# Optimization experiments

Measured on AMD Instinct MI355X. Metric: run time of the kernel, lower is better.

The kernel has to match this reference:

```python
import jax, jax.numpy as jnp
import numpy as np

B, T, C, H, HS = 4, 2048, 1024, 16, 64
EPS = 1e-5


def setup_inputs() -> dict:
    key = jax.random.key(0)
    ks = jax.random.split(key, 16)
    s = lambda k, shp, fan: jax.random.normal(k, shp, jnp.float32) * (fan ** -0.5)
    return {
        "x": jax.random.normal(ks[0], (B, T, C), jnp.float32),
        "wq": s(ks[1], (H, C, HS), C), "bq": jnp.zeros((H, HS), jnp.float32),
        "wk": s(ks[2], (H, C, HS), C), "bk": jnp.zeros((H, HS), jnp.float32),
        "wv": s(ks[3], (H, C, HS), C), "bv": jnp.zeros((H, HS), jnp.float32),
        "wp": s(ks[4], (C, C), C), "bp": jnp.zeros((C,), jnp.float32),
        "w1": s(ks[5], (C, 4 * C), C), "b1": jnp.zeros((4 * C,), jnp.float32),
        "w2": s(ks[6], (4 * C, C), 4 * C), "b2": jnp.zeros((C,), jnp.float32),
        "g1": jnp.ones((C,), jnp.float32), "be1": jnp.zeros((C,), jnp.float32),
        "g2": jnp.ones((C,), jnp.float32), "be2": jnp.zeros((C,), jnp.float32),
    }


def _layernorm(x, g, b):
    mu = jnp.mean(x, axis=-1, keepdims=True)
    var = jnp.mean(jnp.square(x - mu), axis=-1, keepdims=True)
    return (x - mu) * jax.lax.rsqrt(var + EPS) * g + b


def reference(x, wq, bq, wk, bk, wv, bv, wp, bp, w1, b1, w2, b2, g1, be1, g2, be2):
    Bc, Tc, Cc = x.shape
    h = _layernorm(x, g1, be1)
    # per-head projections stacked: [B,H,T,HS]
    q = jnp.einsum('btc,hcd->bhtd', h, wq) + bq[None, :, None, :]
    k = jnp.einsum('btc,hcd->bhtd', h, wk) + bk[None, :, None, :]
    v = jnp.einsum('btc,hcd->bhtd', h, wv) + bv[None, :, None, :]
    # NOTE: source scales by 1/sqrt(n_embd), not 1/sqrt(head_size)
    scores = jnp.einsum('bhtd,bhsd->bhts', q, k) * (Cc ** -0.5)
    causal = jnp.tril(jnp.ones((Tc, Tc), bool))
    scores = jnp.where(causal, scores, -jnp.inf)
    attn = jax.nn.softmax(scores, axis=-1)
    out = jnp.einsum('bhts,bhsd->bhtd', attn, v)
    out = out.transpose(0, 2, 1, 3).reshape(Bc, Tc, Cc)  # concat heads
    x = x + out @ wp + bp
    h2 = _layernorm(x, g2, be2)
    ffn = jax.nn.relu(h2 @ w1 + b1) @ w2 + b2
    return x + ffn
```

## Files before the change

### kernel.cpp

```cpp
#include <hip/hip_runtime.h>


constexpr int Bb = 4, Tt = 2048, Cc = 1024, Hh = 16, HSz = 64, Ff = 4096;
constexpr int Mrows = Bb * Tt;

typedef __attribute__((ext_vector_type(8))) short bf16x8;
typedef __attribute__((ext_vector_type(4))) float f32x4;

__device__ __forceinline__ ushort f2bf(float f) {
  uint u = __builtin_bit_cast(uint, f);
  uint r = (u + 0x7fffu + ((u >> 16) & 1u)) >> 16;
  return (ushort)r;
}
__device__ __forceinline__ float bf2f(ushort s) {
  return __builtin_bit_cast(float, ((uint)s) << 16);
}
__device__ __forceinline__ uint cvtpk_bf16(float lo, float hi) {
  uint r;
  asm("v_cvt_pk_bf16_f32 %0, %1, %2" : "=v"(r) : "v"(lo), "v"(hi));
  return r;
}
__device__ __forceinline__ void gload16(const void* g, void* l) {
  __builtin_amdgcn_global_load_lds(
      (const __attribute__((address_space(1))) void*)g,
      (__attribute__((address_space(3))) void*)l, 16, 0, 0);
}

__global__ __launch_bounds__(256) void ln_kernel(const float* __restrict__ x,
                                                 const float* __restrict__ g,
                                                 const float* __restrict__ b,
                                                 ushort* __restrict__ out) {
  int row = blockIdx.x;
  const float* xr = x + (size_t)row * Cc;
  int c4 = threadIdx.x * 4;
  float4 v = *(const float4*)(xr + c4);
  float s1 = v.x + v.y + v.z + v.w;
  float s2 = v.x * v.x + v.y * v.y + v.z * v.z + v.w * v.w;
#pragma unroll
  for (int off = 32; off >= 1; off >>= 1) {
    s1 += __shfl_xor(s1, off);
    s2 += __shfl_xor(s2, off);
  }
  __shared__ float red[8];
  int wid = threadIdx.x >> 6, lane = threadIdx.x & 63;
  if (lane == 0) { red[wid] = s1; red[4 + wid] = s2; }
  __syncthreads();
  float t1 = red[0] + red[1] + red[2] + red[3];
  float t2 = red[4] + red[5] + red[6] + red[7];
  float mu = t1 * (1.0f / Cc);
  float var = t2 * (1.0f / Cc) - mu * mu;
  float rs = rsqrtf(var + 1e-5f);
  float4 gv = *(const float4*)(g + c4);
  float4 bv = *(const float4*)(b + c4);
  ushort4 o;
  o.x = f2bf((v.x - mu) * rs * gv.x + bv.x);
  o.y = f2bf((v.y - mu) * rs * gv.y + bv.y);
  o.z = f2bf((v.z - mu) * rs * gv.z + bv.z);
  o.w = f2bf((v.w - mu) * rs * gv.w + bv.w);
  *(ushort4*)(out + (size_t)row * Cc + c4) = o;
}

__device__ __forceinline__ void tcast_body(const float* __restrict__ src,
                                           ushort* __restrict__ dst, int ldS,
                                           int ldD, int r0, int c0) {
  __shared__ float t[32][33];
  int c = threadIdx.x & 31, r8 = threadIdx.x >> 5;
#pragma unroll
  for (int i = 0; i < 4; ++i) {
    int r = r8 + i * 8;
    t[r][c] = src[(size_t)(r0 + r) * ldS + c0 + c];
  }
  __syncthreads();
#pragma unroll
  for (int i = 0; i < 4; ++i) {
    int rr = r8 + i * 8;
    dst[(size_t)(c0 + rr) * ldD + r0 + c] = f2bf(t[c][rr]);
  }
}

__global__ __launch_bounds__(256) void tcast_kernel(const float* __restrict__ src,
                                                    ushort* __restrict__ dst,
                                                    int ldS, int ldD) {
  tcast_body(src, dst, ldS, ldD, blockIdx.x * 32, blockIdx.y * 32);
}

__global__ __launch_bounds__(256) void tcast_qkv(const float* __restrict__ wq,
                                                 const float* __restrict__ wk,
                                                 const float* __restrict__ wv,
                                                 ushort* __restrict__ dst) {
  int z = blockIdx.z, zz = z >> 4, h = z & 15;
  const float* src = (zz == 0 ? wq : (zz == 1 ? wk : wv)) + (size_t)h * Cc * HSz;
  ushort* d = dst + (size_t)(zz * 1024 + h * 64) * 1024;
  tcast_body(src, d, HSz, Cc, blockIdx.x * 32, blockIdx.y * 32);
}

__global__ __launch_bounds__(256) void bias_concat(const float* __restrict__ bq,
                                                   const float* __restrict__ bk,
                                                   const float* __restrict__ bv,
                                                   float* __restrict__ dst) {
  int i = blockIdx.x * 256 + threadIdx.x;
  dst[i] = i < 1024 ? bq[i] : (i < 2048 ? bk[i - 1024] : bv[i - 2048]);
}

__device__ __forceinline__ void gemm_main(const ushort* __restrict__ A, int lda,
                                          const ushort* __restrict__ Bt, int ldb,
                                          int K, int m0, int n0,
                                          ushort* __restrict__ As,
                                          ushort* __restrict__ Bs,
                                          f32x4 (&acc)[4][2]) {
  int tid = threadIdx.x, wid = tid >> 6, lane = tid & 63;
  int wr = wid >> 2, wc = wid & 3, fr = lane & 15, fq = lane >> 4;
  const ushort* Ag = A + (size_t)m0 * lda;
  const ushort* Bg = Bt + (size_t)n0 * ldb;
  for (int k0 = 0; k0 < K; k0 += 64) {
#pragma unroll
    for (int c = 0; c < 2; ++c) {
      int slot = c * 512 + tid;
      int row = slot >> 3, s = slot & 7;
      int sw = (s << 3) ^ ((row & 7) << 3);
      gload16(Ag + (size_t)row * lda + k0 + sw, As + (size_t)(c * 512 + wid * 64) * 8);
      gload16(Bg + (size_t)row * ldb + k0 + sw, Bs + (size_t)(c * 512 + wid * 64) * 8);
    }
    __syncthreads();
    bf16x8 av[4][2], bv[2][2];
#pragma unroll
    for (int m = 0; m < 4; ++m) {
      int row = wr * 64 + m * 16 + fr;
#pragma unroll
      for (int ks = 0; ks < 2; ++ks)
        av[m][ks] = *(const bf16x8*)&As[row * 64 + (((ks * 4 + fq) ^ (row & 7)) << 3)];
    }
#pragma unroll
    for (int n = 0; n < 2; ++n) {
      int row = wc * 32 + n * 16 + fr;
#pragma unroll
      for (int ks = 0; ks < 2; ++ks)
        bv[n][ks] = *(const bf16x8*)&Bs[row * 64 + (((ks * 4 + fq) ^ (row & 7)) << 3)];
    }
#pragma unroll
    for (int m = 0; m < 4; ++m)
#pragma unroll
      for (int n = 0; n < 2; ++n)
#pragma unroll
        for (int ks = 0; ks < 2; ++ks)
          acc[m][n] = __builtin_amdgcn_mfma_f32_16x16x32_bf16(
              av[m][ks], bv[n][ks], acc[m][n], 0, 0, 0);
    __syncthreads();
  }
}

__device__ __forceinline__ void xcd_swz(int& bx, int& by) {
  int bid = blockIdx.x + blockIdx.y * gridDim.x;
  int cpx = (gridDim.x * gridDim.y) >> 3;
  int id = (bid & 7) * cpx + (bid >> 3);
  bx = id % gridDim.x;
  by = id / gridDim.x;
}

template <bool RELU, bool HASRES, bool OUTBF16>
__global__ __launch_bounds__(512) void gemm_bf16(
    const ushort* __restrict__ A, int lda, const ushort* __restrict__ Bt,
    int ldb, const float* __restrict__ bias, const float* __restrict__ res,
    void* __restrict__ Cout, int ldc, int K) {
  __shared__ __align__(16) ushort As[128 * 64];
  __shared__ __align__(16) ushort Bs[128 * 64];
  f32x4 acc[4][2] = {};
  int bx, by;
  xcd_swz(bx, by);
  int m0 = by * 128, n0 = bx * 128;
  gemm_main(A, lda, Bt, ldb, K, m0, n0, As, Bs, acc);
  int lane = threadIdx.x & 63, wid = threadIdx.x >> 6;
  int wr = wid >> 2, wc = wid & 3, fr = lane & 15, fq = lane >> 4;
#pragma unroll
  for (int m = 0; m < 4; ++m) {
    int gm = m0 + wr * 64 + m * 16 + fq * 4;
#pragma unroll
    for (int n = 0; n < 2; ++n) {
      int gn = n0 + wc * 32 + n * 16 + fr;
      float bsv = bias[gn];
#pragma unroll
      for (int j = 0; j < 4; ++j) {
        int row = gm + j;
        float v = acc[m][n][j] + bsv;
        if constexpr (HASRES) v += res[(size_t)row * ldc + gn];
        if constexpr (RELU) v = fmaxf(v, 0.f);
        if constexpr (OUTBF16)
          ((ushort*)Cout)[(size_t)row * ldc + gn] = f2bf(v);
        else
          ((float*)Cout)[(size_t)row * ldc + gn] = v;
      }
    }
  }
}

__global__ __launch_bounds__(512) void gemm_qkv(const ushort* __restrict__ A,
                                                const ushort* __restrict__ Bt,
                                                const float* __restrict__ bias,
                                                ushort* __restrict__ q,
                                                ushort* __restrict__ k,
                                                ushort* __restrict__ vt) {
  __shared__ __align__(16) ushort As[128 * 64];
  __shared__ __align__(16) ushort Bs[128 * 64];
  f32x4 acc[4][2] = {};
  int bx, by;
  xcd_swz(bx, by);
  int m0 = by * 128, n0 = bx * 128;
  gemm_main(A, 1024, Bt, 1024, 1024, m0, n0, As, Bs, acc);
  int lane = threadIdx.x & 63, wid = threadIdx.x >> 6;
  int wr = wid >> 2, wc = wid & 3, fr = lane & 15, fq = lane >> 4;
  const float qscale = 1.4426950408889634f / 32.0f;
#pragma unroll
  for (int m = 0; m < 4; ++m) {
    int gm = m0 + wr * 64 + m * 16 + fq * 4;
#pragma unroll
    for (int n = 0; n < 2; ++n) {
      int gn = n0 + wc * 32 + n * 16 + fr;
      float bsv = bias[gn];
      if (gn < 1024) {
#pragma unroll
        for (int j = 0; j < 4; ++j)
          q[(size_t)(gm + j) * 1024 + gn] = f2bf((acc[m][n][j] + bsv) * qscale);
      } else if (gn < 2048) {
        int col = gn - 1024;
#pragma unroll
        for (int j = 0; j < 4; ++j)
          k[(size_t)(gm + j) * 1024 + col] = f2bf(acc[m][n][j] + bsv);
      } else {
        int dd = gn - 2048, h = dd >> 6, d = dd & 63;
        int bbr = gm >> 11, t = gm & 2047;
        ushort4 pw = {f2bf(acc[m][n][0] + bsv), f2bf(acc[m][n][1] + bsv),
                      f2bf(acc[m][n][2] + bsv), f2bf(acc[m][n][3] + bsv)};
        *(ushort4*)&vt[(((size_t)(bbr * 16 + h)) * 64 + d) * 2048 + t] = pw;
      }
    }
  }
}

constexpr int QB = 128, KVB = 64;
__global__ __launch_bounds__(512) void attn_kernel(const ushort* __restrict__ Qb,
                                                   const ushort* __restrict__ Kb,
                                                   const ushort* __restrict__ Vt,
                                                   ushort* __restrict__ att) {
  __shared__ __align__(16) ushort Klds[2][64 * 64];
  __shared__ __align__(16) ushort Vlds[2][64 * 64];
  __shared__ __align__(16) ushort Plds[8][16 * 64];
  int tid = threadIdx.x, wid = tid >> 6, lane = tid & 63;
  int fr = lane & 15, fq = lane >> 4;
  int bh = blockIdx.y, bb = bh >> 4, hh = bh & 15;
  const ushort* qkbase = Qb + ((size_t)bb * Tt) * Cc + hh * HSz;
  const ushort* Kbase = Kb + ((size_t)bb * Tt) * Cc + hh * HSz;
  const ushort* Vbase = Vt + ((size_t)(bb * Hh + hh)) * HSz * Tt;
  int srow = tid >> 3;
  int ssw = ((tid & 7) << 3) ^ ((srow & 7) << 3);

#pragma unroll 1
  for (int pass = 0; pass < 2; ++pass) {
    int qt = pass ? (Tt / QB - 1 - (int)blockIdx.x) : (int)blockIdx.x;
    int q0 = qt * QB;
    int q0w = q0 + wid * 16;

    bf16x8 Qreg[2];
#pragma unroll
    for (int d2 = 0; d2 < 2; ++d2)
      Qreg[d2] = *(const bf16x8*)(qkbase + (size_t)(q0w + fr) * Cc + d2 * 32 + fq * 8);
    f32x4 Oa[4] = {};
    float mrow = -1e30f, lrow = 0.f;
    int nt = q0 / KVB + 2;

    __syncthreads();
    gload16(Kbase + (size_t)srow * Cc + ssw, (char*)Klds[0] + wid * 1024);
    gload16(Vbase + (size_t)srow * Tt + ssw, (char*)Vlds[0] + wid * 1024);

#pragma unroll 1
    for (int kt = 0; kt < nt; ++kt) {
      int t0 = kt * KVB;
      int c = kt & 1;
      __syncthreads();
      if (kt + 1 < nt) {
        int t0n = t0 + KVB;
        gload16(Kbase + (size_t)(t0n + srow) * Cc + ssw,
                (char*)Klds[c ^ 1] + wid * 1024);
        gload16(Vbase + (size_t)srow * Tt + t0n + ssw,
                (char*)Vlds[c ^ 1] + wid * 1024);
      }
      if (q0w + 15 < t0) continue;

      const char* Kc = (const char*)Klds[c];
      const char* Vc = (const char*)Vlds[c];
      bf16x8 kf[4][2];
#pragma unroll
      for (int ks = 0; ks < 4; ++ks)
#pragma unroll
        for (int d2 = 0; d2 < 2; ++d2) {
          int row = ks * 16 + fr;
          int off = (d2 * 64 + fq * 16) ^ ((row & 7) << 4);
          kf[ks][d2] = *(const bf16x8*)(Kc + row * 128 + off);
        }
      f32x4 accs[4] = {};
      __builtin_amdgcn_s_setprio(1);
#pragma unroll
      for (int ks = 0; ks < 4; ++ks) {
        accs[ks] = __builtin_amdgcn_mfma_f32_16x16x32_bf16(
            kf[ks][0], Qreg[0], accs[ks], 0, 0, 0);
        accs[ks] = __builtin_amdgcn_mfma_f32_16x16x32_bf16(
            kf[ks][1], Qreg[1], accs[ks], 0, 0, 0);
      }
      __builtin_amdgcn_s_setprio(0);

      float sv[4][4];
      float vmax = -1e30f;
      if (t0 + 63 <= q0w) {
#pragma unroll
        for (int ks = 0; ks < 4; ++ks)
#pragma unroll
          for (int j = 0; j < 4; ++j) {
            sv[ks][j] = accs[ks][j];
            vmax = fmaxf(vmax, sv[ks][j]);
          }
      } else {
        int qg = q0w + fr;
#pragma unroll
        for (int ks = 0; ks < 4; ++ks)
#pragma unroll
          for (int j = 0; j < 4; ++j) {
            int kg = t0 + ks * 16 + fq * 4 + j;
            float s = accs[ks][j];
            s = (kg <= qg) ? s : -1e30f;
            sv[ks][j] = s;
            vmax = fmaxf(vmax, s);
          }
      }
      float mnew = mrow;
      if (!__all(vmax <= mrow + 11.0f)) {
        float rmax = fmaxf(vmax, __shfl_xor(vmax, 16));
        rmax = fmaxf(rmax, __shfl_xor(rmax, 32));
        mnew = fmaxf(mrow, rmax);
        float sf = exp2f(mrow - mnew);
        mrow = mnew;
        lrow *= sf;
#pragma unroll
        for (int j = 0; j < 4; ++j) {
          float sfo = __shfl(sf, fq * 4 + j);
#pragma unroll
          for (int ds = 0; ds < 4; ++ds) Oa[ds][j] *= sfo;
        }
      }
      char* pbase = (char*)Plds[wid] + fr * 128;
#pragma unroll
      for (int ks = 0; ks < 4; ++ks) {
        float p0 = exp2f(sv[ks][0] - mnew);
        float p1 = exp2f(sv[ks][1] - mnew);
        float p2 = exp2f(sv[ks][2] - mnew);
        float p3 = exp2f(sv[ks][3] - mnew);
        lrow += (p0 + p1) + (p2 + p3);
        uint2 pw = {cvtpk_bf16(p0, p1), cvtpk_bf16(p2, p3)};
        int off = (ks * 32 + fq * 8) ^ ((fr & 7) << 4);
        *(uint2*)(pbase + off) = pw;
      }

      bf16x8 vf[4][2];
#pragma unroll
      for (int ds = 0; ds < 4; ++ds)
#pragma unroll
        for (int k2 = 0; k2 < 2; ++k2) {
          int row = ds * 16 + fr;
          int off = (k2 * 64 + fq * 16) ^ ((row & 7) << 4);
          vf[ds][k2] = *(const bf16x8*)(Vc + row * 128 + off);
        }
      bf16x8 pf[2];
#pragma unroll
      for (int k2 = 0; k2 < 2; ++k2) {
        int off = (k2 * 64 + fq * 16) ^ ((fr & 7) << 4);
        pf[k2] = *(const bf16x8*)((const char*)Plds[wid] + fr * 128 + off);
      }
      __builtin_amdgcn_s_setprio(1);
#pragma unroll
      for (int ds = 0; ds < 4; ++ds) {
        Oa[ds] = __builtin_amdgcn_mfma_f32_16x16x32_bf16(
            pf[0], vf[ds][0], Oa[ds], 0, 0, 0);
        Oa[ds] = __builtin_amdgcn_mfma_f32_16x16x32_bf16(
            pf[1], vf[ds][1], Oa[ds], 0, 0, 0);
      }
      __builtin_amdgcn_s_setprio(0);
    }

    {
      lrow += __shfl_xor(lrow, 16);
      lrow += __shfl_xor(lrow, 32);
      float linv = 1.f / lrow;
#pragma unroll
      for (int j = 0; j < 4; ++j) {
        float lo = __shfl(linv, fq * 4 + j);
        int qg = q0w + fq * 4 + j;
        ushort* orow = att + (size_t)(bb * Tt + qg) * Cc + hh * HSz;
#pragma unroll
        for (int ds = 0; ds < 4; ++ds)
          orow[ds * 16 + fr] = f2bf(Oa[ds][j] * lo);
      }
    }
  }
}

extern "C" void kernel_launch(void* const* d_in, const int* in_sizes, int n_in,
                              void* d_out, int out_size, void* d_ws,
                              size_t ws_size, hipStream_t stream) {
  const float* x = (const float*)d_in[0];
  const float* wq = (const float*)d_in[1];
  const float* bq = (const float*)d_in[2];
  const float* wk = (const float*)d_in[3];
  const float* bk = (const float*)d_in[4];
  const float* wv = (const float*)d_in[5];
  const float* bv = (const float*)d_in[6];
  const float* wp = (const float*)d_in[7];
  const float* bp = (const float*)d_in[8];
  const float* w1 = (const float*)d_in[9];
  const float* b1 = (const float*)d_in[10];
  const float* w2 = (const float*)d_in[11];
  const float* b2 = (const float*)d_in[12];
  const float* g1 = (const float*)d_in[13];
  const float* be1 = (const float*)d_in[14];
  const float* g2 = (const float*)d_in[15];
  const float* be2 = (const float*)d_in[16];
  float* out = (float*)d_out;

  ushort* Qb = (ushort*)d_ws;
  ushort* Kb = Qb + (size_t)8388608;
  ushort* Vt = Kb + (size_t)8388608;
  ushort* att = Vt + (size_t)8388608;
  ushort* ffh = Qb;
  ushort* h1b = att + (size_t)8388608;
  float* x2 = (float*)(h1b + (size_t)8388608);
  ushort* wqkvT = (ushort*)(x2 + (size_t)8388608);
  ushort* wpT = wqkvT + (size_t)3145728;
  ushort* w1T = wpT + (size_t)1048576;
  ushort* w2T = w1T + (size_t)4194304;
  float* bqkv = (float*)(w2T + (size_t)4194304);

  tcast_qkv<<<dim3(32, 2, 48), 256, 0, stream>>>(wq, wk, wv, wqkvT);
  tcast_kernel<<<dim3(32, 32), 256, 0, stream>>>(wp, wpT, 1024, 1024);
  tcast_kernel<<<dim3(32, 128), 256, 0, stream>>>(w1, w1T, 4096, 1024);
  tcast_kernel<<<dim3(128, 32), 256, 0, stream>>>(w2, w2T, 1024, 4096);
  bias_concat<<<dim3(12), 256, 0, stream>>>(bq, bk, bv, bqkv);

  ln_kernel<<<dim3(Mrows), 256, 0, stream>>>(x, g1, be1, h1b);
  gemm_qkv<<<dim3(24, 64), 512, 0, stream>>>(h1b, wqkvT, bqkv, Qb, Kb, Vt);
  attn_kernel<<<dim3(Tt / QB / 2, Bb * Hh), 512, 0, stream>>>(Qb, Kb, Vt, att);
  gemm_bf16<false, true, false><<<dim3(8, 64), 512, 0, stream>>>(
      att, 1024, wpT, 1024, bp, x, x2, 1024, 1024);
  ln_kernel<<<dim3(Mrows), 256, 0, stream>>>(x2, g2, be2, h1b);
  gemm_bf16<true, false, true><<<dim3(32, 64), 512, 0, stream>>>(
      h1b, 1024, w1T, 1024, b1, nullptr, ffh, 4096, 1024);
  gemm_bf16<false, true, false><<<dim3(8, 64), 512, 0, stream>>>(
      ffh, 4096, w2T, 4096, b2, x2, out, 1024, 4096);
}
```

Before: 368.0 us.

## Use 256x256 double-buffered ping-pong GEMM for QKV and FFN1 projections

```diff
diff --git a/kernel.cpp b/kernel.cpp
--- a/kernel.cpp
+++ b/kernel.cpp
@@ -25,6 +25,13 @@
       (const __attribute__((address_space(1))) void*)g,
       (__attribute__((address_space(3))) void*)l, 16, 0, 0);
 }
+#define VMCNT0 asm volatile("s_waitcnt vmcnt(0)" ::: "memory")
+#define LGKM0                                        \
+  do {                                               \
+    asm volatile("s_waitcnt lgkmcnt(0)" ::: "memory"); \
+    __builtin_amdgcn_sched_barrier(0);               \
+  } while (0)
+#define BARRIER __builtin_amdgcn_s_barrier()
 
 __global__ __launch_bounds__(256) void ln_kernel(const float* __restrict__ x,
                                                  const float* __restrict__ g,
@@ -102,6 +109,178 @@
   dst[i] = i < 1024 ? bq[i] : (i < 2048 ? bk[i - 1024] : bv[i - 2048]);
 }
 
+__device__ __forceinline__ void xcd_swz(int& bx, int& by) {
+  int bid = blockIdx.x + blockIdx.y * gridDim.x;
+  int cpx = (gridDim.x * gridDim.y) >> 3;
+  int id = (bid & 7) * cpx + (bid >> 3);
+  bx = id % gridDim.x;
+  by = id / gridDim.x;
+}
+
+template <int MH, int NH>
+__device__ __forceinline__ void mfma16(f32x4 (&acc)[8][4], bf16x8 (&a)[4][2],
+                                       bf16x8 (&b)[2][2]) {
+#pragma unroll
+  for (int m = 0; m < 4; ++m)
+#pragma unroll
+    for (int n = 0; n < 2; ++n)
+#pragma unroll
+      for (int kk = 0; kk < 2; ++kk)
+        acc[MH * 4 + m][NH * 2 + n] = __builtin_amdgcn_mfma_f32_16x16x32_bf16(
+            a[m][kk], b[n][kk], acc[MH * 4 + m][NH * 2 + n], 0, 0, 0);
+}
+
+__device__ __forceinline__ void gemm256_main(const ushort* __restrict__ A,
+                                             const ushort* __restrict__ Bt,
+                                             int m0, int n0,
+                                             ushort* __restrict__ As,
+                                             ushort* __restrict__ Bs,
+                                             f32x4 (&acc)[8][4]) {
+  constexpr int NKT = 16;
+  int tid = threadIdx.x, wid = tid >> 6, lane = tid & 63;
+  int wr = wid >> 2, wc = wid & 3, fr = lane & 15, fq = lane >> 4;
+  const ushort* Ag = A + (size_t)m0 * 1024;
+  const ushort* Bg = Bt + (size_t)n0 * 1024;
+  int r0 = tid >> 3, r1 = 64 + (tid >> 3);
+  int sc = ((tid & 7) ^ ((tid >> 3) & 7)) << 3;
+
+  auto stage = [&](int ktn, int h, int ns) {
+    const ushort* g = (h < 2) ? Ag : Bg;
+    ushort* l = ((h < 2) ? As : Bs) + ns * 16384 + (h & 1) * 8192;
+    int kcol = ktn * 64, rbase = (h & 1) * 128;
+    gload16(g + (size_t)(rbase + r0) * 1024 + kcol + sc, l + (size_t)wid * 512);
+    gload16(g + (size_t)(rbase + r1) * 1024 + kcol + sc,
+            l + (size_t)(512 + wid * 64) * 8);
+  };
+  auto readA = [&](int slot, int mh, bf16x8 (&a)[4][2]) {
+#pragma unroll
+    for (int m = 0; m < 4; ++m) {
+      int row = wr * 128 + mh * 64 + m * 16 + fr;
+#pragma unroll
+      for (int kk = 0; kk < 2; ++kk)
+        a[m][kk] = *(const bf16x8*)&As[slot * 16384 + row * 64 +
+                                       (((kk * 4 + fq) ^ (row & 7)) << 3)];
+    }
+  };
+  auto readB = [&](int slot, int nh, bf16x8 (&b)[2][2]) {
+#pragma unroll
+    for (int n = 0; n < 2; ++n) {
+      int row = wc * 64 + nh * 32 + n * 16 + fr;
+#pragma unroll
+      for (int kk = 0; kk < 2; ++kk)
+        b[n][kk] = *(const bf16x8*)&Bs[slot * 16384 + row * 64 +
+                                       (((kk * 4 + fq) ^ (row & 7)) << 3)];
+    }
+  };
+
+  stage(0, 0, 0); stage(0, 1, 0); stage(0, 2, 0); stage(0, 3, 0);
+  VMCNT0;
+  BARRIER;
+
+  bf16x8 a[4][2], b0[2][2], b1[2][2];
+#pragma unroll 1
+  for (int kt = 0; kt < NKT; ++kt) {
+    int slot = kt & 1, ns = slot ^ 1;
+    bool st = (kt + 1 < NKT);
+    readA(slot, 0, a);
+    readB(slot, 0, b0);
+    if (st) { stage(kt + 1, 0, ns); stage(kt + 1, 2, ns); }
+    BARRIER;
+    LGKM0;
+    __builtin_amdgcn_s_setprio(1);
+    mfma16<0, 0>(acc, a, b0);
+    __builtin_amdgcn_s_setprio(0);
+    BARRIER;
+    readB(slot, 1, b1);
+    if (st) { stage(kt + 1, 1, ns); stage(kt + 1, 3, ns); }
+    BARRIER;
+    LGKM0;
+    __builtin_amdgcn_s_setprio(1);
+    mfma16<0, 1>(acc, a, b1);
+    __builtin_amdgcn_s_setprio(0);
+    BARRIER;
+    readA(slot, 1, a);
+    BARRIER;
+    LGKM0;
+    __builtin_amdgcn_s_setprio(1);
+    mfma16<1, 0>(acc, a, b0);
+    __builtin_amdgcn_s_setprio(0);
+    BARRIER;
+    __builtin_amdgcn_s_setprio(1);
+    mfma16<1, 1>(acc, a, b1);
+    __builtin_amdgcn_s_setprio(0);
+    VMCNT0;
+    BARRIER;
+  }
+}
+
+__global__ __launch_bounds__(512, 2) void gemm256_relu(
+    const ushort* __restrict__ A, const ushort* __restrict__ Bt,
+    const float* __restrict__ bias, ushort* __restrict__ Cout, int ldc) {
+  __shared__ __align__(16) ushort As[2 * 256 * 64];
+  __shared__ __align__(16) ushort Bs[2 * 256 * 64];
+  f32x4 acc[8][4] = {};
+  int bx, by;
+  xcd_swz(bx, by);
+  int m0 = by * 256, n0 = bx * 256;
+  gemm256_main(A, Bt, m0, n0, As, Bs, acc);
+  int lane = threadIdx.x & 63, wid = threadIdx.x >> 6;
+  int wr = wid >> 2, wc = wid & 3, fr = lane & 15, fq = lane >> 4;
+#pragma unroll
+  for (int i = 0; i < 8; ++i) {
+    int gm = m0 + wr * 128 + (i >> 2) * 64 + (i & 3) * 16 + fq * 4;
+#pragma unroll
+    for (int j2 = 0; j2 < 4; ++j2) {
+      int gn = n0 + wc * 64 + (j2 >> 1) * 32 + (j2 & 1) * 16 + fr;
+      float bsv = bias[gn];
+#pragma unroll
+      for (int j = 0; j < 4; ++j)
+        Cout[(size_t)(gm + j) * ldc + gn] = f2bf(fmaxf(acc[i][j2][j] + bsv, 0.f));
+    }
+  }
+}
+
+__global__ __launch_bounds__(512, 2) void gemm256_qkv(
+    const ushort* __restrict__ A, const ushort* __restrict__ Bt,
+    const float* __restrict__ bias, ushort* __restrict__ q,
+    ushort* __restrict__ k, ushort* __restrict__ vt) {
+  __shared__ __align__(16) ushort As[2 * 256 * 64];
+  __shared__ __align__(16) ushort Bs[2 * 256 * 64];
+  f32x4 acc[8][4] = {};
+  int bx, by;
+  xcd_swz(bx, by);
+  int m0 = by * 256, n0 = bx * 256;
+  gemm256_main(A, Bt, m0, n0, As, Bs, acc);
+  int lane = threadIdx.x & 63, wid = threadIdx.x >> 6;
+  int wr = wid >> 2, wc = wid & 3, fr = lane & 15, fq = lane >> 4;
+  const float qscale = 1.4426950408889634f / 32.0f;
+#pragma unroll
+  for (int i = 0; i < 8; ++i) {
+    int gm = m0 + wr * 128 + (i >> 2) * 64 + (i & 3) * 16 + fq * 4;
+#pragma unroll
+    for (int j2 = 0; j2 < 4; ++j2) {
+      int gn = n0 + wc * 64 + (j2 >> 1) * 32 + (j2 & 1) * 16 + fr;
+      float bsv = bias[gn];
+      if (gn < 1024) {
+#pragma unroll
+        for (int j = 0; j < 4; ++j)
+          q[(size_t)(gm + j) * 1024 + gn] = f2bf((acc[i][j2][j] + bsv) * qscale);
+      } else if (gn < 2048) {
+        int col = gn - 1024;
+#pragma unroll
+        for (int j = 0; j < 4; ++j)
+          k[(size_t)(gm + j) * 1024 + col] = f2bf(acc[i][j2][j] + bsv);
+      } else {
+        int dd = gn - 2048, h = dd >> 6, d = dd & 63;
+        int bbr = gm >> 11, t = gm & 2047;
+        ushort4 pw = {f2bf(acc[i][j2][0] + bsv), f2bf(acc[i][j2][1] + bsv),
+                      f2bf(acc[i][j2][2] + bsv), f2bf(acc[i][j2][3] + bsv)};
+        *(ushort4*)&vt[(((size_t)(bbr * 16 + h)) * 64 + d) * 2048 + t] = pw;
+      }
+    }
+  }
+}
+
 __device__ __forceinline__ void gemm_main(const ushort* __restrict__ A, int lda,
                                           const ushort* __restrict__ Bt, int ldb,
                                           int K, int m0, int n0,
@@ -147,14 +326,6 @@
               av[m][ks], bv[n][ks], acc[m][n], 0, 0, 0);
     __syncthreads();
   }
-}
-
-__device__ __forceinline__ void xcd_swz(int& bx, int& by) {
-  int bid = blockIdx.x + blockIdx.y * gridDim.x;
-  int cpx = (gridDim.x * gridDim.y) >> 3;
-  int id = (bid & 7) * cpx + (bid >> 3);
-  bx = id % gridDim.x;
-  by = id / gridDim.x;
 }
 
 template <bool RELU, bool HASRES, bool OUTBF16>
@@ -188,49 +359,6 @@
           ((ushort*)Cout)[(size_t)row * ldc + gn] = f2bf(v);
         else
           ((float*)Cout)[(size_t)row * ldc + gn] = v;
-      }
-    }
-  }
-}
-
-__global__ __launch_bounds__(512) void gemm_qkv(const ushort* __restrict__ A,
-                                                const ushort* __restrict__ Bt,
-                                                const float* __restrict__ bias,
-                                                ushort* __restrict__ q,
-                                                ushort* __restrict__ k,
-                                                ushort* __restrict__ vt) {
-  __shared__ __align__(16) ushort As[128 * 64];
-  __shared__ __align__(16) ushort Bs[128 * 64];
-  f32x4 acc[4][2] = {};
-  int bx, by;
-  xcd_swz(bx, by);
-  int m0 = by * 128, n0 = bx * 128;
-  gemm_main(A, 1024, Bt, 1024, 1024, m0, n0, As, Bs, acc);
-  int lane = threadIdx.x & 63, wid = threadIdx.x >> 6;
-  int wr = wid >> 2, wc = wid & 3, fr = lane & 15, fq = lane >> 4;
-  const float qscale = 1.4426950408889634f / 32.0f;
-#pragma unroll
-  for (int m = 0; m < 4; ++m) {
-    int gm = m0 + wr * 64 + m * 16 + fq * 4;
-#pragma unroll
-    for (int n = 0; n < 2; ++n) {
-      int gn = n0 + wc * 32 + n * 16 + fr;
-      float bsv = bias[gn];
-      if (gn < 1024) {
-#pragma unroll
-        for (int j = 0; j < 4; ++j)
-          q[(size_t)(gm + j) * 1024 + gn] = f2bf((acc[m][n][j] + bsv) * qscale);
-      } else if (gn < 2048) {
-        int col = gn - 1024;
-#pragma unroll
-        for (int j = 0; j < 4; ++j)
-          k[(size_t)(gm + j) * 1024 + col] = f2bf(acc[m][n][j] + bsv);
-      } else {
-        int dd = gn - 2048, h = dd >> 6, d = dd & 63;
-        int bbr = gm >> 11, t = gm & 2047;
-        ushort4 pw = {f2bf(acc[m][n][0] + bsv), f2bf(acc[m][n][1] + bsv),
-                      f2bf(acc[m][n][2] + bsv), f2bf(acc[m][n][3] + bsv)};
-        *(ushort4*)&vt[(((size_t)(bbr * 16 + h)) * 64 + d) * 2048 + t] = pw;
       }
     }
   }
@@ -443,13 +571,12 @@
   bias_concat<<<dim3(12), 256, 0, stream>>>(bq, bk, bv, bqkv);
 
   ln_kernel<<<dim3(Mrows), 256, 0, stream>>>(x, g1, be1, h1b);
-  gemm_qkv<<<dim3(24, 64), 512, 0, stream>>>(h1b, wqkvT, bqkv, Qb, Kb, Vt);
+  gemm256_qkv<<<dim3(12, 32), 512, 0, stream>>>(h1b, wqkvT, bqkv, Qb, Kb, Vt);
   attn_kernel<<<dim3(Tt / QB / 2, Bb * Hh), 512, 0, stream>>>(Qb, Kb, Vt, att);
   gemm_bf16<false, true, false><<<dim3(8, 64), 512, 0, stream>>>(
       att, 1024, wpT, 1024, bp, x, x2, 1024, 1024);
   ln_kernel<<<dim3(Mrows), 256, 0, stream>>>(x2, g2, be2, h1b);
-  gemm_bf16<true, false, true><<<dim3(32, 64), 512, 0, stream>>>(
-      h1b, 1024, w1T, 1024, b1, nullptr, ffh, 4096, 1024);
+  gemm256_relu<<<dim3(16, 32), 512, 0, stream>>>(h1b, w1T, b1, ffh, 4096);
   gemm_bf16<false, true, false><<<dim3(8, 64), 512, 0, stream>>>(
       ffh, 4096, w2T, 4096, b2, x2, out, 1024, 4096);
 }
```

Result: faster. 358.2 us (-2.6%).
